# Kernel tuning notes

Hardware: AMD Instinct MI355X
Metric: run time of the kernel (lower is better)

Reference implementation:

```python
import jax, jax.numpy as jnp
import numpy as np

WS = 8          # window size (square)
GRID_H = 64     # patch grid height
GRID_W = 64     # patch grid width
B = 16          # batch
C = 256         # features per token
NH = 8          # heads
HD = C // NH    # head dim
NL = 2          # blocks in stage (plain + shifted)
N = WS * WS     # tokens per window
MLP_HID = 4 * C
CPB_HID = 512   # hidden width of continuous position-bias MLP


def _rel_index(ws):
    # standard swin relative position index, (N*N,) into (2ws-1)^2 table
    coords = np.stack(np.meshgrid(np.arange(ws), np.arange(ws), indexing='ij')).reshape(2, -1)
    rel = (coords[:, :, None] - coords[:, None, :]).transpose(1, 2, 0) + (ws - 1)  # (N,N,2)
    idx = rel[..., 0] * (2 * ws - 1) + rel[..., 1]
    return idx.reshape(-1).astype(np.int32)


def _rel_table(ws):
    # swinv2 log-spaced relative coords table, ((2ws-1)^2, 2)
    r = np.arange(-(ws - 1), ws, dtype=np.float32)
    tab = np.stack(np.meshgrid(r, r, indexing='ij'), -1)  # (2ws-1, 2ws-1, 2)
    tab = tab / (ws - 1) * 8.0  # pretrained_window_size=None -> normalize by window_size-1
    tab = np.sign(tab) * np.log2(np.abs(tab) + 1.0) / np.log2(8.0)
    return tab.reshape(-1, 2).astype(np.float32)


def _shift_mask(H, W, ws, shift):
    # (num_windows, N, N) additive mask with -100 between shifted regions
    img = np.zeros((H, W), np.int32)
    cnt = 0
    for hs in (slice(0, H - ws), slice(H - ws, H - shift), slice(H - shift, H)):
        for vs in (slice(0, W - ws), slice(W - ws, W - shift), slice(W - shift, W)):
            img[hs, vs] = cnt
            cnt += 1
    win = img.reshape(H // ws, ws, W // ws, ws).transpose(0, 2, 1, 3).reshape(-1, ws * ws)
    diff = win[:, None, :] != win[:, :, None]
    return np.where(diff, -100.0, 0.0).astype(np.float32)


REL_IDX = jnp.asarray(_rel_index(WS))
REL_TAB = jnp.asarray(_rel_table(WS))


def setup_inputs() -> dict:
    key = jax.random.key(0)
    ks = jax.random.split(key, 8)
    rn = lambda k, shape, s=0.02: jax.random.normal(k, shape, jnp.float32) * s
    return dict(
        tokens=jax.random.normal(ks[0], (B, GRID_H * GRID_W, C), jnp.float32),
        grid_h=GRID_H,
        grid_w=GRID_W,
        qkv_w=rn(ks[1], (NL, 3 * C, C)),
        qkv_b=jnp.zeros((NL, 3 * C), jnp.float32),
        logit_scale=jnp.full((NL, NH, 1, 1), np.log(10.0), jnp.float32),
        cpb_w1=rn(ks[2], (NL, CPB_HID, 2), 0.1),
        cpb_b1=jnp.zeros((NL, CPB_HID), jnp.float32),
        cpb_w2=rn(ks[3], (NL, NH, CPB_HID), 0.1),
        proj_w=rn(ks[4], (NL, C, C)),
        proj_b=jnp.zeros((NL, C), jnp.float32),
        norm1_s=jnp.ones((NL, C), jnp.float32),
        norm1_b=jnp.zeros((NL, C), jnp.float32),
        mlp_w1=rn(ks[5], (NL, MLP_HID, C)),
        mlp_b1=jnp.zeros((NL, MLP_HID), jnp.float32),
        mlp_w2=rn(ks[6], (NL, C, MLP_HID)),
        mlp_b2=jnp.zeros((NL, C), jnp.float32),
        norm2_s=jnp.ones((NL, C), jnp.float32),
        norm2_b=jnp.zeros((NL, C), jnp.float32),
    )


def _layernorm(x, s, b):
    m = jnp.mean(x, -1, keepdims=True)
    v = jnp.mean(jnp.square(x - m), -1, keepdims=True)
    return (x - m) * jax.lax.rsqrt(v + 1e-5) * s + b


def _window_attn(x, H, W, shift, qkv_w, qkv_b, logit_scale, cpb_w1, cpb_b1, cpb_w2, proj_w, proj_b):
    Bt = x.shape[0]
    x = x.reshape(Bt, H, W, C)
    if shift > 0:
        x = jnp.roll(x, (-shift, -shift), axis=(1, 2))
    nwh, nww = H // WS, W // WS
    # window partition: (Bt*nwh*nww, N, C)
    xw = x.reshape(Bt, nwh, WS, nww, WS, C).transpose(0, 1, 3, 2, 4, 5).reshape(-1, N, C)
    qkv = (xw @ qkv_w.T + qkv_b).reshape(-1, N, 3, NH, HD).transpose(2, 0, 3, 1, 4)
    q, k, v = qkv[0], qkv[1], qkv[2]  # (BW, NH, N, HD)
    # swinv2 scaled cosine attention
    q = q / (jnp.linalg.norm(q, axis=-1, keepdims=True) + 1e-12)
    k = k / (jnp.linalg.norm(k, axis=-1, keepdims=True) + 1e-12)
    scale = jnp.exp(jnp.minimum(logit_scale, jnp.log(100.0)))  # (NH,1,1)
    attn = jnp.einsum('bhnd,bhmd->bhnm', q, k) * scale
    # continuous relative position bias MLP
    cpb = jax.nn.relu(REL_TAB @ cpb_w1.T + cpb_b1) @ cpb_w2.T  # (M, NH)
    bias = 16.0 * jax.nn.sigmoid(cpb[REL_IDX].reshape(N, N, NH).transpose(2, 0, 1))
    attn = attn + bias
    if shift > 0:
        mask = jnp.asarray(_shift_mask(H, W, WS, shift))  # (nwin, N, N)
        nwin = mask.shape[0]
        attn = (attn.reshape(Bt, nwin, NH, N, N) + mask[None, :, None]).reshape(-1, NH, N, N)
    attn = jax.nn.softmax(attn, axis=-1)
    out = jnp.einsum('bhnm,bhmd->bhnd', attn, v).transpose(0, 2, 1, 3).reshape(-1, N, C)
    out = out @ proj_w.T + proj_b
    # window un-partition
    out = out.reshape(Bt, nwh, nww, WS, WS, C).transpose(0, 1, 3, 2, 4, 5).reshape(Bt, H, W, C)
    if shift > 0:
        out = jnp.roll(out, (shift, shift), axis=(1, 2))
    return out.reshape(Bt, H * W, C)


def reference(tokens, grid_h, grid_w, qkv_w, qkv_b, logit_scale, cpb_w1, cpb_b1, cpb_w2,
              proj_w, proj_b, norm1_s, norm1_b, mlp_w1, mlp_b1, mlp_w2, mlp_b2,
              norm2_s, norm2_b):
    x = tokens
    for i in range(NL):
        shift = 0 if i % 2 == 0 else WS // 2  # even blocks plain, odd blocks shifted
        a = _window_attn(x, grid_h, grid_w, shift, qkv_w[i], qkv_b[i], logit_scale[i],
                         cpb_w1[i], cpb_b1[i], cpb_w2[i], proj_w[i], proj_b[i])
        a = _layernorm(a, norm1_s[i], norm1_b[i])  # swinv2 post-norm
        x = x + a
        m = jax.nn.gelu(x @ mlp_w1[i].T + mlp_b1[i], approximate=False) @ mlp_w2[i].T + mlp_b2[i]
        m = _layernorm(m, norm2_s[i], norm2_b[i])
        x = x + m
    return x
```

## Files before the change

### kernel.cpp

```cpp
#include <hip/hip_runtime.h>
#include <math.h>

#define C_    256
#define NTOK  65536
#define HWIN  512

#define AP_LDS  (4*64*72*2 + 64*256*2)
#define MLP_LDS (64*264*4)

typedef __bf16 bf16x8 __attribute__((ext_vector_type(8)));
typedef float  f32x4  __attribute__((ext_vector_type(4)));
#define MFMA16(a,b,c) __builtin_amdgcn_mfma_f32_16x16x32_bf16((a),(b),(c),0,0,0)

__device__ inline ushort f2b(float f) {
    unsigned u = __builtin_bit_cast(unsigned, f);
    return (ushort)((u + 0x7fffu + ((u >> 16) & 1u)) >> 16);
}

union BF8u { ushort u[8]; bf16x8 v; };
__device__ inline bf16x8 cvt8(float4 a, float4 b) {
    BF8u t;
    t.u[0] = f2b(a.x); t.u[1] = f2b(a.y); t.u[2] = f2b(a.z); t.u[3] = f2b(a.w);
    t.u[4] = f2b(b.x); t.u[5] = f2b(b.y); t.u[6] = f2b(b.z); t.u[7] = f2b(b.w);
    return t.v;
}

__global__ void f2b_kernel(ushort* __restrict__ dst, const float* __restrict__ src) {
    size_t i = ((size_t)blockIdx.x * 256 + threadIdx.x) * 4;
    float4 v = *reinterpret_cast<const float4*>(src + i);
    ushort4 u = { f2b(v.x), f2b(v.y), f2b(v.z), f2b(v.w) };
    *reinterpret_cast<ushort4*>(dst + i) = u;
}

__global__ void cpb_kernel(const float* __restrict__ w1, const float* __restrict__ b1,
                           const float* __restrict__ w2, float* __restrict__ biastab) {
    __shared__ float red[256];
    const int e = blockIdx.x;
    const int t = threadIdx.x;
    const int p = e / 15, q = e % 15;
    const float v0 = (float)(p - 7) * (8.0f / 7.0f);
    const float v1 = (float)(q - 7) * (8.0f / 7.0f);
    const float t0 = copysignf(log2f(fabsf(v0) + 1.0f) * (1.0f / 3.0f), v0);
    const float t1 = copysignf(log2f(fabsf(v1) + 1.0f) * (1.0f / 3.0f), v1);
    const float ha = fmaxf(0.0f, t0 * w1[t * 2]         + t1 * w1[t * 2 + 1]         + b1[t]);
    const float hb = fmaxf(0.0f, t0 * w1[(t + 256) * 2] + t1 * w1[(t + 256) * 2 + 1] + b1[t + 256]);
    for (int h = 0; h < 8; ++h) {
        __syncthreads();
        red[t] = ha * w2[h * 512 + t] + hb * w2[h * 512 + t + 256];
        __syncthreads();
        for (int s = 128; s > 0; s >>= 1) {
            if (t < s) red[t] += red[t + s];
            __syncthreads();
        }
        if (t == 0) biastab[e * 8 + h] = 16.0f / (1.0f + expf(-red[0]));
    }
}

__global__ void biasx_kernel(const float* __restrict__ biastab, float* __restrict__ biasx) {
    int h = blockIdx.x >> 6, n = blockIdx.x & 63, m = threadIdx.x;
    int idx = ((n >> 3) - (m >> 3) + 7) * 15 + ((n & 7) - (m & 7) + 7);
    biasx[((size_t)(h * 64 + n)) * 64 + m] = biastab[idx * 8 + h];
}

__global__ __launch_bounds__(256, 3) void qkv_kernel(
    const float* __restrict__ x, const ushort* __restrict__ qwb,
    const float* __restrict__ qb, ushort* __restrict__ q_ws,
    ushort* __restrict__ k_ws, ushort* __restrict__ vT_ws,
    int shift, int win0)
{
    __shared__ ushort xs[64 * 256];
    const int t = threadIdx.x;
    const int win = win0 + blockIdx.x, lwin = blockIdx.x;
    const int b = win >> 6, wh = (win >> 3) & 7, ww = win & 7;
    const int w = t >> 6, l = t & 63, lr = l & 15, lg = l >> 4;
    const int aswz = (lr & 7) << 3;
    const f32x4 zf = { 0.f, 0.f, 0.f, 0.f };

    {
        int row = t >> 2, seg = t & 3;
        int i = row >> 3, j = row & 7;
        int rr = (wh * 8 + i + shift) & 63;
        int cc = (ww * 8 + j + shift) & 63;
        const float* src = x + ((size_t)(b * 4096 + rr * 64 + cc)) * 256 + seg * 64;
        #pragma unroll
        for (int k8 = 0; k8 < 8; ++k8) {
            float4 v0 = *reinterpret_cast<const float4*>(src + k8 * 8);
            float4 v1 = *reinterpret_cast<const float4*>(src + k8 * 8 + 4);
            int col = seg * 64 + k8 * 8;
            *reinterpret_cast<bf16x8*>(xs + row * 256 + (col ^ ((row & 7) << 3))) = cvt8(v0, v1);
        }
    }
    __syncthreads();

    for (int round = 0; round < 3; ++round) {
        const int colb = round * 256 + w * 64;
        f32x4 acc[4][4];
        #pragma unroll
        for (int mf = 0; mf < 4; ++mf)
            #pragma unroll
            for (int nf = 0; nf < 4; ++nf) acc[mf][nf] = zf;

        for (int kt = 0; kt < 8; ++kt) {
            int k0 = kt * 32 + lg * 8;
            bf16x8 a[4], bfr[4];
            #pragma unroll
            for (int mf = 0; mf < 4; ++mf)
                a[mf] = *reinterpret_cast<const bf16x8*>(xs + (mf * 16 + lr) * 256 + (k0 ^ aswz));
            #pragma unroll
            for (int nf = 0; nf < 4; ++nf)
                bfr[nf] = *reinterpret_cast<const bf16x8*>(qwb + (size_t)(colb + nf * 16 + lr) * 256 + k0);
            #pragma unroll
            for (int mf = 0; mf < 4; ++mf)
                #pragma unroll
                for (int nf = 0; nf < 4; ++nf)
                    acc[mf][nf] = MFMA16(a[mf], bfr[nf], acc[mf][nf]);
        }

        #pragma unroll
        for (int nf = 0; nf < 4; ++nf) {
            float bb = qb[colb + nf * 16 + lr];
            #pragma unroll
            for (int mf = 0; mf < 4; ++mf)
                #pragma unroll
                for (int r = 0; r < 4; ++r) acc[mf][nf][r] += bb;
        }

        if (round < 2) {
            float ss0[4][4], ss1[4][4];
            #pragma unroll
            for (int mf = 0; mf < 4; ++mf)
                #pragma unroll
                for (int r = 0; r < 4; ++r) {
                    ss0[mf][r] = acc[mf][0][r] * acc[mf][0][r] + acc[mf][1][r] * acc[mf][1][r];
                    ss1[mf][r] = acc[mf][2][r] * acc[mf][2][r] + acc[mf][3][r] * acc[mf][3][r];
                }
            #pragma unroll
            for (int m = 1; m < 16; m <<= 1)
                #pragma unroll
                for (int mf = 0; mf < 4; ++mf)
                    #pragma unroll
                    for (int r = 0; r < 4; ++r) {
                        ss0[mf][r] += __shfl_xor(ss0[mf][r], m);
                        ss1[mf][r] += __shfl_xor(ss1[mf][r], m);
                    }
            ushort* dst = (round == 0) ? q_ws : k_ws;
            #pragma unroll
            for (int mf = 0; mf < 4; ++mf)
                #pragma unroll
                for (int r = 0; r < 4; ++r) {
                    float rs0 = 1.0f / (sqrtf(ss0[mf][r]) + 1e-12f);
                    float rs1 = 1.0f / (sqrtf(ss1[mf][r]) + 1e-12f);
                    size_t rowoff = ((size_t)lwin * 64 + mf * 16 + lg * 4 + r) * 256;
                    #pragma unroll
                    for (int nf = 0; nf < 4; ++nf)
                        dst[rowoff + w * 64 + nf * 16 + lr] =
                            f2b(acc[mf][nf][r] * (nf < 2 ? rs0 : rs1));
                }
        } else {
            #pragma unroll
            for (int nf = 0; nf < 4; ++nf) {
                int h = 2 * w + (nf >> 1);
                int chan = (nf & 1) * 16 + lr;
                ushort* vrow = vT_ws + (((size_t)lwin * 8 + h) * 32 + chan) * 64;
                #pragma unroll
                for (int mf = 0; mf < 4; ++mf)
                    #pragma unroll
                    for (int r = 0; r < 4; ++r)
                        vrow[mf * 16 + lg * 4 + r] = f2b(acc[mf][nf][r]);
            }
        }
    }
}

__global__ __launch_bounds__(256, 2) void attnproj_kernel(
    const ushort* __restrict__ q_ws, const ushort* __restrict__ k_ws,
    const ushort* __restrict__ vT_ws, const ushort* __restrict__ pwb,
    const float* __restrict__ pb, const float* __restrict__ lsc,
    const float* __restrict__ biasx, const float* __restrict__ n1s,
    const float* __restrict__ n1b, const float* __restrict__ xin,
    float* __restrict__ xout, int shift, int win0)
{
    extern __shared__ ushort sm[];
    ushort* aol  = sm + 4 * 64 * 72;
    float*  outT = (float*)sm;

    const int t = threadIdx.x;
    const int win = win0 + blockIdx.x, lwin = blockIdx.x;
    const int b = win >> 6, wh = (win >> 3) & 7, ww = win & 7;
    const int w = t >> 6, l = t & 63, lr = l & 15, lg = l >> 4;
    ushort* Pw = sm + w * 64 * 72;
    const size_t tokbase = (size_t)lwin * 64;
    const f32x4 zf = { 0.f, 0.f, 0.f, 0.f };

    int regc[4], regr[4][4];
    #pragma unroll
    for (int nf = 0; nf < 4; ++nf) {
        int kc = nf * 16 + lr;
        int pr = wh * 8 + (kc >> 3), pc = ww * 8 + (kc & 7);
        regc[nf] = ((pr < 56) ? 0 : ((pr < 60) ? 1 : 2)) * 3 +
                   ((pc < 56) ? 0 : ((pc < 60) ? 1 : 2));
    }
    #pragma unroll
    for (int mf = 0; mf < 4; ++mf)
        #pragma unroll
        for (int r = 0; r < 4; ++r) {
            int n = mf * 16 + lg * 4 + r;
            int pr = wh * 8 + (n >> 3), pc = ww * 8 + (n & 7);
            regr[mf][r] = ((pr < 56) ? 0 : ((pr < 60) ? 1 : 2)) * 3 +
                          ((pc < 56) ? 0 : ((pc < 60) ? 1 : 2));
        }

    for (int hr = 0; hr < 2; ++hr) {
        const int h = w * 2 + hr;

        f32x4 sacc[4][4];
        {
            bf16x8 aq[4], bk[4];
            #pragma unroll
            for (int mf = 0; mf < 4; ++mf)
                aq[mf] = *reinterpret_cast<const bf16x8*>(
                    q_ws + (tokbase + mf * 16 + lr) * 256 + h * 32 + lg * 8);
            #pragma unroll
            for (int nf = 0; nf < 4; ++nf)
                bk[nf] = *reinterpret_cast<const bf16x8*>(
                    k_ws + (tokbase + nf * 16 + lr) * 256 + h * 32 + lg * 8);
            #pragma unroll
            for (int mf = 0; mf < 4; ++mf)
                #pragma unroll
                for (int nf = 0; nf < 4; ++nf)
                    sacc[mf][nf] = MFMA16(aq[mf], bk[nf], zf);
        }

        const float scale = __expf(fminf(lsc[h], 4.6051702f));
        float mx[4][4], sum[4][4];
        #pragma unroll
        for (int mf = 0; mf < 4; ++mf)
            #pragma unroll
            for (int r = 0; r < 4; ++r) mx[mf][r] = -1e30f;

        #pragma unroll
        for (int nf = 0; nf < 4; ++nf)
            #pragma unroll
            for (int mf = 0; mf < 4; ++mf)
                #pragma unroll
                for (int r = 0; r < 4; ++r) {
                    float v = sacc[mf][nf][r] * scale +
                              biasx[((size_t)(h * 64 + mf * 16 + lg * 4 + r)) * 64 + nf * 16 + lr];
                    if (shift && regc[nf] != regr[mf][r]) v -= 100.0f;
                    sacc[mf][nf][r] = v;
                    mx[mf][r] = fmaxf(mx[mf][r], v);
                }
        #pragma unroll
        for (int m = 1; m < 16; m <<= 1)
            #pragma unroll
            for (int mf = 0; mf < 4; ++mf)
                #pragma unroll
                for (int r = 0; r < 4; ++r) mx[mf][r] = fmaxf(mx[mf][r], __shfl_xor(mx[mf][r], m));

        #pragma unroll
        for (int mf = 0; mf < 4; ++mf)
            #pragma unroll
            for (int r = 0; r < 4; ++r) sum[mf][r] = 0.f;
        #pragma unroll
        for (int nf = 0; nf < 4; ++nf)
            #pragma unroll
            for (int mf = 0; mf < 4; ++mf)
                #pragma unroll
                for (int r = 0; r < 4; ++r) {
                    float e = __expf(sacc[mf][nf][r] - mx[mf][r]);
                    sacc[mf][nf][r] = e;
                    sum[mf][r] += e;
                }
        #pragma unroll
        for (int m = 1; m < 16; m <<= 1)
            #pragma unroll
            for (int mf = 0; mf < 4; ++mf)
                #pragma unroll
                for (int r = 0; r < 4; ++r) sum[mf][r] += __shfl_xor(sum[mf][r], m);

        #pragma unroll
        for (int nf = 0; nf < 4; ++nf)
            #pragma unroll
            for (int mf = 0; mf < 4; ++mf)
                #pragma unroll
                for (int r = 0; r < 4; ++r)
                    Pw[(mf * 16 + lg * 4 + r) * 72 + nf * 16 + lr] = f2b(sacc[mf][nf][r]);

        f32x4 oacc[4][2];
        #pragma unroll
        for (int mf = 0; mf < 4; ++mf)
            #pragma unroll
            for (int nf = 0; nf < 2; ++nf) oacc[mf][nf] = zf;
        #pragma unroll
        for (int ks = 0; ks < 2; ++ks) {
            bf16x8 pa[4], bv[2];
            #pragma unroll
            for (int mf = 0; mf < 4; ++mf)
                pa[mf] = *reinterpret_cast<const bf16x8*>(Pw + (mf * 16 + lr) * 72 + ks * 32 + lg * 8);
            #pragma unroll
            for (int nf = 0; nf < 2; ++nf)
                bv[nf] = *reinterpret_cast<const bf16x8*>(
                    vT_ws + (((size_t)lwin * 8 + h) * 32 + nf * 16 + lr) * 64 + ks * 32 + lg * 8);
            #pragma unroll
            for (int mf = 0; mf < 4; ++mf)
                #pragma unroll
                for (int nf = 0; nf < 2; ++nf)
                    oacc[mf][nf] = MFMA16(pa[mf], bv[nf], oacc[mf][nf]);
        }

        #pragma unroll
        for (int mf = 0; mf < 4; ++mf)
            #pragma unroll
            for (int r = 0; r < 4; ++r) {
                float inv = 1.0f / sum[mf][r];
                int row = mf * 16 + lg * 4 + r;
                #pragma unroll
                for (int nf = 0; nf < 2; ++nf) {
                    int col = h * 32 + nf * 16 + lr;
                    aol[row * 256 + (col ^ ((row & 7) << 3))] = f2b(oacc[mf][nf][r] * inv);
                }
            }
    }
    __syncthreads();

    f32x4 acc[4][4];
    #pragma unroll
    for (int mf = 0; mf < 4; ++mf)
        #pragma unroll
        for (int nf = 0; nf < 4; ++nf) acc[mf][nf] = zf;
    const int aswz = (lr & 7) << 3;
    for (int kt = 0; kt < 8; ++kt) {
        int k0 = kt * 32 + lg * 8;
        bf16x8 a[4], bfr[4];
        #pragma unroll
        for (int mf = 0; mf < 4; ++mf)
            a[mf] = *reinterpret_cast<const bf16x8*>(aol + (mf * 16 + lr) * 256 + (k0 ^ aswz));
        #pragma unroll
        for (int nf = 0; nf < 4; ++nf)
            bfr[nf] = *reinterpret_cast<const bf16x8*>(
                pwb + (size_t)(w * 64 + nf * 16 + lr) * 256 + k0);
        #pragma unroll
        for (int mf = 0; mf < 4; ++mf)
            #pragma unroll
            for (int nf = 0; nf < 4; ++nf)
                acc[mf][nf] = MFMA16(a[mf], bfr[nf], acc[mf][nf]);
    }
    __syncthreads();

    #pragma unroll
    for (int nf = 0; nf < 4; ++nf) {
        int c = w * 64 + nf * 16 + lr;
        float bb = pb[c];
        #pragma unroll
        for (int mf = 0; mf < 4; ++mf)
            #pragma unroll
            for (int r = 0; r < 4; ++r)
                outT[(mf * 16 + lg * 4 + r) * 264 + c] = acc[mf][nf][r] + bb;
    }
    __syncthreads();

    for (int u = 0; u < 16; ++u) {
        int tk = w * 16 + u;
        float v0 = outT[tk * 264 + l];
        float v1 = outT[tk * 264 + l + 64];
        float v2 = outT[tk * 264 + l + 128];
        float v3 = outT[tk * 264 + l + 192];
        float s = v0 + v1 + v2 + v3, ss = v0 * v0 + v1 * v1 + v2 * v2 + v3 * v3;
        for (int m = 1; m < 64; m <<= 1) { s += __shfl_xor(s, m); ss += __shfl_xor(ss, m); }
        float mean = s * (1.0f / 256.0f);
        float var  = ss * (1.0f / 256.0f) - mean * mean;
        float rs   = rsqrtf(var + 1e-5f);

        int i = tk >> 3, j = tk & 7;
        int pr = (wh * 8 + i + shift) & 63;
        int pc = (ww * 8 + j + shift) & 63;
        size_t gaddr = ((size_t)(b * 4096 + pr * 64 + pc)) * 256;
        xout[gaddr + l]       = xin[gaddr + l]       + (v0 - mean) * rs * n1s[l]       + n1b[l];
        xout[gaddr + l + 64]  = xin[gaddr + l + 64]  + (v1 - mean) * rs * n1s[l + 64]  + n1b[l + 64];
        xout[gaddr + l + 128] = xin[gaddr + l + 128] + (v2 - mean) * rs * n1s[l + 128] + n1b[l + 128];
        xout[gaddr + l + 192] = xin[gaddr + l + 192] + (v3 - mean) * rs * n1s[l + 192] + n1b[l + 192];
    }
}

__global__ __launch_bounds__(256, 2) void mlp_mfma_kernel(
    float* __restrict__ x, const ushort* __restrict__ w1b, const float* __restrict__ b1,
    const ushort* __restrict__ w2b, const float* __restrict__ b2,
    const float* __restrict__ n2s, const float* __restrict__ n2b)
{
    extern __shared__ ushort sm2[];
    ushort* xs = sm2;
    ushort* hc = sm2 + 64 * 256;
    float*  outT = (float*)sm2;

    const int t = threadIdx.x;
    const size_t tok0 = (size_t)blockIdx.x * 64;
    const int w = t >> 6, l = t & 63, lr = l & 15, lg = l >> 4;
    const int aswz = (lr & 7) << 3;
    const f32x4 zf = { 0.f, 0.f, 0.f, 0.f };

    {
        int row = t >> 2, seg = t & 3;
        const float* src = x + (tok0 + row) * 256 + seg * 64;
        #pragma unroll
        for (int k8 = 0; k8 < 8; ++k8) {
            float4 v0 = *reinterpret_cast<const float4*>(src + k8 * 8);
            float4 v1 = *reinterpret_cast<const float4*>(src + k8 * 8 + 4);
            int col = seg * 64 + k8 * 8;
            *reinterpret_cast<bf16x8*>(xs + row * 256 + (col ^ ((row & 7) << 3))) = cvt8(v0, v1);
        }
    }
    __syncthreads();

    f32x4 acc2[4][4];
    #pragma unroll
    for (int mf = 0; mf < 4; ++mf)
        #pragma unroll
        for (int nf = 0; nf < 4; ++nf) acc2[mf][nf] = zf;

    for (int c = 0; c < 4; ++c) {
        f32x4 acc1[4][4];
        #pragma unroll
        for (int mf = 0; mf < 4; ++mf)
            #pragma unroll
            for (int nf = 0; nf < 4; ++nf) acc1[mf][nf] = zf;

        const int hcol0 = c * 256 + w * 64;
        for (int kt = 0; kt < 8; ++kt) {
            int k0 = kt * 32 + lg * 8;
            bf16x8 a[4], bfr[4];
            #pragma unroll
            for (int mf = 0; mf < 4; ++mf)
                a[mf] = *reinterpret_cast<const bf16x8*>(xs + (mf * 16 + lr) * 256 + (k0 ^ aswz));
            #pragma unroll
            for (int nf = 0; nf < 4; ++nf)
                bfr[nf] = *reinterpret_cast<const bf16x8*>(
                    w1b + (size_t)(hcol0 + nf * 16 + lr) * 256 + k0);
            #pragma unroll
            for (int mf = 0; mf < 4; ++mf)
                #pragma unroll
                for (int nf = 0; nf < 4; ++nf)
                    acc1[mf][nf] = MFMA16(a[mf], bfr[nf], acc1[mf][nf]);
        }

        __syncthreads();

        #pragma unroll
        for (int nf = 0; nf < 4; ++nf) {
            int lcol = w * 64 + nf * 16 + lr;
            float bb = b1[c * 256 + lcol];
            #pragma unroll
            for (int mf = 0; mf < 4; ++mf)
                #pragma unroll
                for (int r = 0; r < 4; ++r) {
                    int hrow = mf * 16 + lg * 4 + r;
                    float pre = acc1[mf][nf][r] + bb;
                    float g = 0.5f * pre * (1.0f + erff(pre * 0.70710678f));
                    hc[hrow * 256 + (lcol ^ ((hrow & 7) << 3))] = f2b(g);
                }
        }
        __syncthreads();

        for (int kt = 0; kt < 8; ++kt) {
            int k0 = kt * 32 + lg * 8;
            bf16x8 a[4], bfr[4];
            #pragma unroll
            for (int mf = 0; mf < 4; ++mf)
                a[mf] = *reinterpret_cast<const bf16x8*>(hc + (mf * 16 + lr) * 256 + (k0 ^ aswz));
            #pragma unroll
            for (int nf = 0; nf < 4; ++nf)
                bfr[nf] = *reinterpret_cast<const bf16x8*>(
                    w2b + (size_t)(w * 64 + nf * 16 + lr) * 1024 + c * 256 + k0);
            #pragma unroll
            for (int mf = 0; mf < 4; ++mf)
                #pragma unroll
                for (int nf = 0; nf < 4; ++nf)
                    acc2[mf][nf] = MFMA16(a[mf], bfr[nf], acc2[mf][nf]);
        }
    }
    __syncthreads();

    #pragma unroll
    for (int nf = 0; nf < 4; ++nf) {
        int cc = w * 64 + nf * 16 + lr;
        float bb = b2[cc];
        #pragma unroll
        for (int mf = 0; mf < 4; ++mf)
            #pragma unroll
            for (int r = 0; r < 4; ++r)
                outT[(mf * 16 + lg * 4 + r) * 264 + cc] = acc2[mf][nf][r] + bb;
    }
    __syncthreads();

    for (int u = 0; u < 16; ++u) {
        int tk = w * 16 + u;
        float v0 = outT[tk * 264 + l];
        float v1 = outT[tk * 264 + l + 64];
        float v2 = outT[tk * 264 + l + 128];
        float v3 = outT[tk * 264 + l + 192];
        float s = v0 + v1 + v2 + v3, ss = v0 * v0 + v1 * v1 + v2 * v2 + v3 * v3;
        for (int m = 1; m < 64; m <<= 1) { s += __shfl_xor(s, m); ss += __shfl_xor(ss, m); }
        float mean = s * (1.0f / 256.0f);
        float var  = ss * (1.0f / 256.0f) - mean * mean;
        float rs   = rsqrtf(var + 1e-5f);
        float* xp = x + (tok0 + tk) * 256;
        xp[l]       += (v0 - mean) * rs * n2s[l]       + n2b[l];
        xp[l + 64]  += (v1 - mean) * rs * n2s[l + 64]  + n2b[l + 64];
        xp[l + 128] += (v2 - mean) * rs * n2s[l + 128] + n2b[l + 128];
        xp[l + 192] += (v3 - mean) * rs * n2s[l + 192] + n2b[l + 192];
    }
}

extern "C" void kernel_launch(void* const* d_in, const int* in_sizes, int n_in,
                              void* d_out, int out_size, void* d_ws, size_t ws_size,
                              hipStream_t stream) {
    (void)in_sizes; (void)n_in; (void)out_size; (void)ws_size;
    const float* tokens = (const float*)d_in[0];
    const float* qkv_w  = (const float*)d_in[3];
    const float* qkv_b  = (const float*)d_in[4];
    const float* lsc    = (const float*)d_in[5];
    const float* cw1    = (const float*)d_in[6];
    const float* cb1    = (const float*)d_in[7];
    const float* cw2    = (const float*)d_in[8];
    const float* pw     = (const float*)d_in[9];
    const float* pb     = (const float*)d_in[10];
    const float* n1s    = (const float*)d_in[11];
    const float* n1b    = (const float*)d_in[12];
    const float* mw1    = (const float*)d_in[13];
    const float* mb1    = (const float*)d_in[14];
    const float* mw2    = (const float*)d_in[15];
    const float* mb2    = (const float*)d_in[16];
    const float* n2s    = (const float*)d_in[17];
    const float* n2b    = (const float*)d_in[18];

    float* x = (float*)d_out;

    ushort* q_ws  = (ushort*)d_ws;
    ushort* k_ws  = q_ws + (size_t)HWIN * 64 * 256;
    ushort* vT_ws = k_ws + (size_t)HWIN * 64 * 256;
    float*  biastab = (float*)(vT_ws + (size_t)HWIN * 64 * 256);
    ushort* pwb   = (ushort*)((char*)biastab + 7680);
    ushort* w1b   = pwb + 2 * 256 * 256;
    ushort* w2b   = w1b + 2 * 1024 * 256;
    ushort* qwb   = w2b + 2 * 256 * 1024;
    float*  biasx = (float*)(qwb + 2 * 768 * 256);

    f2b_kernel<<<dim3(2 * 256 * 256 / 1024),  dim3(256), 0, stream>>>(pwb, pw);
    f2b_kernel<<<dim3(2 * 1024 * 256 / 1024), dim3(256), 0, stream>>>(w1b, mw1);
    f2b_kernel<<<dim3(2 * 256 * 1024 / 1024), dim3(256), 0, stream>>>(w2b, mw2);
    f2b_kernel<<<dim3(2 * 768 * 256 / 1024),  dim3(256), 0, stream>>>(qwb, qkv_w);

    for (int l = 0; l < 2; ++l) {
        const int shift = l ? 4 : 0;
        const float* xsrc = (l == 0) ? tokens : x;
        cpb_kernel<<<dim3(225), dim3(256), 0, stream>>>(
            cw1 + (size_t)l * 1024, cb1 + (size_t)l * 512, cw2 + (size_t)l * 4096, biastab);
        biasx_kernel<<<dim3(512), dim3(64), 0, stream>>>(biastab, biasx);
        for (int half = 0; half < 2; ++half) {
            qkv_kernel<<<dim3(HWIN), dim3(256), 0, stream>>>(
                xsrc, qwb + (size_t)l * 196608, qkv_b + (size_t)l * 768,
                q_ws, k_ws, vT_ws, shift, half * HWIN);
            attnproj_kernel<<<dim3(HWIN), dim3(256), AP_LDS, stream>>>(
                q_ws, k_ws, vT_ws, pwb + (size_t)l * 65536, pb + (size_t)l * 256,
                lsc + (size_t)l * 8, biasx, n1s + (size_t)l * 256, n1b + (size_t)l * 256,
                xsrc, x, shift, half * HWIN);
        }
        mlp_mfma_kernel<<<dim3(NTOK / 64), dim3(256), MLP_LDS, stream>>>(
            x, w1b + (size_t)l * 262144, mb1 + (size_t)l * 1024,
            w2b + (size_t)l * 262144, mb2 + (size_t)l * 256,
            n2s + (size_t)l * 256, n2b + (size_t)l * 256);
    }
}
```

Before: 877.2 us.

## Split fused MLP into two GEMM kernels with global bf16 hidden buffer

Replaces the fused MLP kernel, which kept the GELU hidden chunk in LDS, with two kernels. The first computes fc1 plus GELU and writes the bf16 hidden activations to a workspace buffer. The second runs fc2 with the residual layernorm epilogue. Token chunking is chosen from the available workspace size, and the hidden buffer aliases the q/k/v workspace. The aim is to remove the LDS round trips and barriers inside the fused loop, at the cost of extra global traffic for the hidden tensor (up to 128MB written and read per layer) and extra launches.

```diff
diff --git a/kernel.cpp b/kernel.cpp
--- a/kernel.cpp
+++ b/kernel.cpp
@@ -5,8 +5,8 @@
 #define NTOK  65536
 #define HWIN  512
 
-#define AP_LDS  (4*64*72*2 + 64*256*2)
-#define MLP_LDS (64*264*4)
+#define AP_LDS   (4*64*72*2 + 64*256*2)
+#define MLP2_LDS (64*264*4)
 
 typedef __bf16 bf16x8 __attribute__((ext_vector_type(8)));
 typedef float  f32x4  __attribute__((ext_vector_type(4)));
@@ -382,18 +382,14 @@
     }
 }
 
-__global__ __launch_bounds__(256, 2) void mlp_mfma_kernel(
-    float* __restrict__ x, const ushort* __restrict__ w1b, const float* __restrict__ b1,
-    const ushort* __restrict__ w2b, const float* __restrict__ b2,
-    const float* __restrict__ n2s, const float* __restrict__ n2b)
+__global__ __launch_bounds__(256, 2) void mlp1_kernel(
+    const float* __restrict__ x, const ushort* __restrict__ w1b,
+    const float* __restrict__ b1, ushort* __restrict__ hidb, int tok_base)
 {
-    extern __shared__ ushort sm2[];
-    ushort* xs = sm2;
-    ushort* hc = sm2 + 64 * 256;
-    float*  outT = (float*)sm2;
-
+    __shared__ ushort xs[64 * 256];
     const int t = threadIdx.x;
-    const size_t tok0 = (size_t)blockIdx.x * 64;
+    const size_t ltok0 = (size_t)blockIdx.x * 64;
+    const size_t tok0  = (size_t)tok_base + ltok0;
     const int w = t >> 6, l = t & 63, lr = l & 15, lg = l >> 4;
     const int aswz = (lr & 7) << 3;
     const f32x4 zf = { 0.f, 0.f, 0.f, 0.f };
@@ -411,20 +407,14 @@
     }
     __syncthreads();
 
-    f32x4 acc2[4][4];
-    #pragma unroll
-    for (int mf = 0; mf < 4; ++mf)
-        #pragma unroll
-        for (int nf = 0; nf < 4; ++nf) acc2[mf][nf] = zf;
-
-    for (int c = 0; c < 4; ++c) {
-        f32x4 acc1[4][4];
-        #pragma unroll
-        for (int mf = 0; mf < 4; ++mf)
-            #pragma unroll
-            for (int nf = 0; nf < 4; ++nf) acc1[mf][nf] = zf;
-
-        const int hcol0 = c * 256 + w * 64;
+    for (int q = 0; q < 4; ++q) {
+        const int n0 = q * 256 + w * 64;
+        f32x4 acc[4][4];
+        #pragma unroll
+        for (int mf = 0; mf < 4; ++mf)
+            #pragma unroll
+            for (int nf = 0; nf < 4; ++nf) acc[mf][nf] = zf;
+
         for (int kt = 0; kt < 8; ++kt) {
             int k0 = kt * 32 + lg * 8;
             bf16x8 a[4], bfr[4];
@@ -434,60 +424,74 @@
             #pragma unroll
             for (int nf = 0; nf < 4; ++nf)
                 bfr[nf] = *reinterpret_cast<const bf16x8*>(
-                    w1b + (size_t)(hcol0 + nf * 16 + lr) * 256 + k0);
+                    w1b + (size_t)(n0 + nf * 16 + lr) * 256 + k0);
             #pragma unroll
             for (int mf = 0; mf < 4; ++mf)
                 #pragma unroll
                 for (int nf = 0; nf < 4; ++nf)
-                    acc1[mf][nf] = MFMA16(a[mf], bfr[nf], acc1[mf][nf]);
-        }
-
-        __syncthreads();
+                    acc[mf][nf] = MFMA16(a[mf], bfr[nf], acc[mf][nf]);
+        }
 
         #pragma unroll
         for (int nf = 0; nf < 4; ++nf) {
-            int lcol = w * 64 + nf * 16 + lr;
-            float bb = b1[c * 256 + lcol];
+            int hcol = n0 + nf * 16 + lr;
+            float bb = b1[hcol];
             #pragma unroll
             for (int mf = 0; mf < 4; ++mf)
                 #pragma unroll
                 for (int r = 0; r < 4; ++r) {
-                    int hrow = mf * 16 + lg * 4 + r;
-                    float pre = acc1[mf][nf][r] + bb;
+                    float pre = acc[mf][nf][r] + bb;
                     float g = 0.5f * pre * (1.0f + erff(pre * 0.70710678f));
-                    hc[hrow * 256 + (lcol ^ ((hrow & 7) << 3))] = f2b(g);
+                    hidb[(ltok0 + mf * 16 + lg * 4 + r) * 1024 + hcol] = f2b(g);
                 }
         }
-        __syncthreads();
-
-        for (int kt = 0; kt < 8; ++kt) {
-            int k0 = kt * 32 + lg * 8;
-            bf16x8 a[4], bfr[4];
-            #pragma unroll
-            for (int mf = 0; mf < 4; ++mf)
-                a[mf] = *reinterpret_cast<const bf16x8*>(hc + (mf * 16 + lr) * 256 + (k0 ^ aswz));
+    }
+}
+
+__global__ __launch_bounds__(256, 2) void mlp2_kernel(
+    const ushort* __restrict__ hidb, const ushort* __restrict__ w2b,
+    const float* __restrict__ b2, const float* __restrict__ n2s,
+    const float* __restrict__ n2b, float* __restrict__ x, int tok_base)
+{
+    extern __shared__ float outT[];
+    const int t = threadIdx.x;
+    const size_t ltok0 = (size_t)blockIdx.x * 64;
+    const size_t tok0  = (size_t)tok_base + ltok0;
+    const int w = t >> 6, l = t & 63, lr = l & 15, lg = l >> 4;
+    const f32x4 zf = { 0.f, 0.f, 0.f, 0.f };
+
+    f32x4 acc[4][4];
+    #pragma unroll
+    for (int mf = 0; mf < 4; ++mf)
+        #pragma unroll
+        for (int nf = 0; nf < 4; ++nf) acc[mf][nf] = zf;
+
+    for (int kt = 0; kt < 32; ++kt) {
+        int k0 = kt * 32 + lg * 8;
+        bf16x8 a[4], bfr[4];
+        #pragma unroll
+        for (int mf = 0; mf < 4; ++mf)
+            a[mf] = *reinterpret_cast<const bf16x8*>(hidb + (ltok0 + mf * 16 + lr) * 1024 + k0);
+        #pragma unroll
+        for (int nf = 0; nf < 4; ++nf)
+            bfr[nf] = *reinterpret_cast<const bf16x8*>(
+                w2b + (size_t)(w * 64 + nf * 16 + lr) * 1024 + k0);
+        #pragma unroll
+        for (int mf = 0; mf < 4; ++mf)
             #pragma unroll
             for (int nf = 0; nf < 4; ++nf)
-                bfr[nf] = *reinterpret_cast<const bf16x8*>(
-                    w2b + (size_t)(w * 64 + nf * 16 + lr) * 1024 + c * 256 + k0);
-            #pragma unroll
-            for (int mf = 0; mf < 4; ++mf)
-                #pragma unroll
-                for (int nf = 0; nf < 4; ++nf)
-                    acc2[mf][nf] = MFMA16(a[mf], bfr[nf], acc2[mf][nf]);
-        }
-    }
-    __syncthreads();
+                acc[mf][nf] = MFMA16(a[mf], bfr[nf], acc[mf][nf]);
+    }
 
     #pragma unroll
     for (int nf = 0; nf < 4; ++nf) {
-        int cc = w * 64 + nf * 16 + lr;
-        float bb = b2[cc];
+        int c = w * 64 + nf * 16 + lr;
+        float bb = b2[c];
         #pragma unroll
         for (int mf = 0; mf < 4; ++mf)
             #pragma unroll
             for (int r = 0; r < 4; ++r)
-                outT[(mf * 16 + lg * 4 + r) * 264 + cc] = acc2[mf][nf][r] + bb;
+                outT[(mf * 16 + lg * 4 + r) * 264 + c] = acc[mf][nf][r] + bb;
     }
     __syncthreads();
 
@@ -513,7 +517,7 @@
 extern "C" void kernel_launch(void* const* d_in, const int* in_sizes, int n_in,
                               void* d_out, int out_size, void* d_ws, size_t ws_size,
                               hipStream_t stream) {
-    (void)in_sizes; (void)n_in; (void)out_size; (void)ws_size;
+    (void)in_sizes; (void)n_in; (void)out_size;
     const float* tokens = (const float*)d_in[0];
     const float* qkv_w  = (const float*)d_in[3];
     const float* qkv_b  = (const float*)d_in[4];
@@ -534,15 +538,23 @@
 
     float* x = (float*)d_out;
 
-    ushort* q_ws  = (ushort*)d_ws;
-    ushort* k_ws  = q_ws + (size_t)HWIN * 64 * 256;
-    ushort* vT_ws = k_ws + (size_t)HWIN * 64 * 256;
-    float*  biastab = (float*)(vT_ws + (size_t)HWIN * 64 * 256);
-    ushort* pwb   = (ushort*)((char*)biastab + 7680);
+    ushort* pwb   = (ushort*)d_ws;
     ushort* w1b   = pwb + 2 * 256 * 256;
     ushort* w2b   = w1b + 2 * 1024 * 256;
     ushort* qwb   = w2b + 2 * 256 * 1024;
     float*  biasx = (float*)(qwb + 2 * 768 * 256);
+    float*  biastab = biasx + 8 * 64 * 64;
+    char*   big   = (char*)d_ws + 3407872;
+
+    ushort* q_ws  = (ushort*)big;
+    ushort* k_ws  = q_ws + (size_t)HWIN * 64 * 256;
+    ushort* vT_ws = k_ws + (size_t)HWIN * 64 * 256;
+    ushort* hidb  = (ushort*)big;
+
+    size_t avail = ws_size - 3407872;
+    int chunk_tok = 16384;
+    if (avail >= (size_t)65536 * 2048)      chunk_tok = 65536;
+    else if (avail >= (size_t)32768 * 2048) chunk_tok = 32768;
 
     f2b_kernel<<<dim3(2 * 256 * 256 / 1024),  dim3(256), 0, stream>>>(pwb, pw);
     f2b_kernel<<<dim3(2 * 1024 * 256 / 1024), dim3(256), 0, stream>>>(w1b, mw1);
@@ -564,9 +576,12 @@
                 lsc + (size_t)l * 8, biasx, n1s + (size_t)l * 256, n1b + (size_t)l * 256,
                 xsrc, x, shift, half * HWIN);
         }
-        mlp_mfma_kernel<<<dim3(NTOK / 64), dim3(256), MLP_LDS, stream>>>(
-            x, w1b + (size_t)l * 262144, mb1 + (size_t)l * 1024,
-            w2b + (size_t)l * 262144, mb2 + (size_t)l * 256,
-            n2s + (size_t)l * 256, n2b + (size_t)l * 256);
-    }
-}
+        for (int tb = 0; tb < NTOK; tb += chunk_tok) {
+            mlp1_kernel<<<dim3(chunk_tok / 64), dim3(256), 0, stream>>>(
+                x, w1b + (size_t)l * 262144, mb1 + (size_t)l * 1024, hidb, tb);
+            mlp2_kernel<<<dim3(chunk_tok / 64), dim3(256), MLP2_LDS, stream>>>(
+                hidb, w2b + (size_t)l * 262144, mb2 + (size_t)l * 256,
+                n2s + (size_t)l * 256, n2b + (size_t)l * 256, x, tb);
+        }
+    }
+}
```

After: 1.071 ms. +22.0%, slower.
